# Performance work log

Hardware: AMD Instinct MI355X
Metric: run time of the kernel (lower is better)

## Reference

```python
import jax, jax.numpy as jnp
import numpy as np

VOCAB = 31      # 29 label chars + EOS('$') + PAD('%')
EMB = 512
KEY_DIM = 512
VAL_DIM = 512
HID = 512
T_ENC = 16384
MAX_LEN = 100
EOS_IDX = 29
PAD_IDX = 30


def setup_inputs() -> dict:
    key = jax.random.key(0)
    ks = jax.random.split(key, 9)
    inp = {
        "encoding": jax.random.normal(ks[0], (1, T_ENC, KEY_DIM + VAL_DIM), jnp.float32),
        "encoding_lens": jnp.array([T_ENC], dtype=jnp.int64),
        # learned parameters
        "embed": jax.random.normal(ks[1], (VOCAB, EMB), jnp.float32) * 0.02,
        "w_ih": jax.random.normal(ks[2], (3 * HID, EMB), jnp.float32) / np.sqrt(EMB),
        "w_hh": jax.random.normal(ks[3], (3 * HID, HID), jnp.float32) / np.sqrt(HID),
        "b_ih": jax.random.normal(ks[4], (3 * HID,), jnp.float32) * 0.01,
        "b_hh": jax.random.normal(ks[5], (3 * HID,), jnp.float32) * 0.01,
        "w_out": jax.random.normal(ks[6], (VOCAB, VAL_DIM + HID), jnp.float32) / np.sqrt(VAL_DIM + HID),
        "b_out": jax.random.normal(ks[7], (VOCAB,), jnp.float32) * 0.01,
    }
    return inp


def _gru_cell(x, h, w_ih, w_hh, b_ih, b_hh):
    # torch.nn.GRUCell math. x: [B,E], h: [B,H]
    gx = x @ w_ih.T + b_ih            # [B,3H]
    gh = h @ w_hh.T + b_hh            # [B,3H]
    r = jax.nn.sigmoid(gx[:, :HID] + gh[:, :HID])
    z = jax.nn.sigmoid(gx[:, HID:2 * HID] + gh[:, HID:2 * HID])
    n = jnp.tanh(gx[:, 2 * HID:] + r * gh[:, 2 * HID:])
    return (1.0 - z) * n + z * h


def reference(encoding, encoding_lens, embed, w_ih, w_hh, b_ih, b_hh, w_out, b_out):
    # batch_size == 1 inference path
    keys = encoding[0, :, :KEY_DIM]     # [T, K]
    values = encoding[0, :, KEY_DIM:]   # [T, V]
    # mask: positions whose key features are not all equal to the pad index
    mask = jnp.any(keys != jnp.float32(PAD_IDX), axis=-1)  # [T]
    scale = 1.0 / np.sqrt(KEY_DIM)

    y0 = embed[EOS_IDX][None, :]        # [1, E]
    h0 = jnp.zeros((1, HID), jnp.float32)

    def step(carry, _):
        y_prev, h = carry
        h_new = _gru_cell(y_prev, h, w_ih, w_hh, b_ih, b_hh)          # [1,H]
        scores = (h_new @ keys.T) * scale                              # [1,T]
        scores = jnp.where(mask[None, :], scores, jnp.float32(-1e9))
        attn = jax.nn.softmax(scores, axis=-1)                         # [1,T]
        summary = attn @ values                                        # [1,V]
        logits = jnp.concatenate([summary, h_new], axis=-1) @ w_out.T + b_out  # [1,VOCAB]
        best = jnp.argmax(logits, axis=-1)                             # [1] (softmax argmax == logits argmax)
        y_next = embed[best]                                           # [1,E]
        return (y_next, h_new), (logits[0], attn[0], best[0])

    _, (outputs, attentions, best_seq) = jax.lax.scan(step, (y0, h0), None, length=MAX_LEN)
    # emulate the early-exit: length = index of first EOS (outputs[:t] in torch), else MAX_LEN
    eos_hit = best_seq == EOS_IDX
    length = jnp.where(eos_hit.any(), jnp.argmax(eos_hit), MAX_LEN).astype(jnp.int32)
    return outputs[None, :, :], length[None], attentions[None, :, :]
```

## Files before the change

kernel.cpp:

```cpp
#include <hip/hip_runtime.h>
#include <math.h>

#define HID 512
#define TENC 16384
#define NBLK 256
#define TPB 512
#define KPB 64
#define NGRP 32
#define GRPSZ 8
#define VOCAB 31
#define EOSI 29
#define MAXLEN 100
#define SCALE 0.044194173824159216f

#define WS_GX    0
#define WS_GH    47616
#define WS_LT    50688
#define WS_BAR   51504

#define OUT_LEN_IDX 3100
#define OUT_ATT_BASE 3101

#define AL(p)    __hip_atomic_load((p), __ATOMIC_RELAXED, __HIP_MEMORY_SCOPE_AGENT)
#define AS(p, v) __hip_atomic_store((p), (v), __ATOMIC_RELAXED, __HIP_MEMORY_SCOPE_AGENT)

static __device__ __forceinline__ float wsum(float v) {
#pragma unroll
  for (int m = 32; m >= 1; m >>= 1) v += __shfl_xor(v, m, 64);
  return v;
}
static __device__ __forceinline__ float sigm(float x) { return 1.0f / (1.0f + expf(-x)); }

__global__ __launch_bounds__(1024) void k_init(const float* __restrict__ b_hh,
                                               float* __restrict__ ws) {
  int idx = blockIdx.x * 1024 + threadIdx.x;
  int* bars = (int*)ws + WS_BAR;
  if (idx < 12832) bars[idx] = 0;
  if (idx < 1536) ws[WS_GH + idx] = b_hh[idx];
  if (idx < 816) ws[WS_LT + idx] = 0.0f;
}

__global__ __launch_bounds__(256) void k_gx_all(const float* __restrict__ embed,
                                                const float* __restrict__ w_ih,
                                                const float* __restrict__ b_ih,
                                                float* __restrict__ ws) {
  int w = threadIdx.x >> 6, lane = threadIdx.x & 63;
  int r = blockIdx.x * 4 + w;
  float wr[8];
  const float* wp = w_ih + (size_t)r * HID + lane * 8;
#pragma unroll
  for (int j = 0; j < 8; ++j) wr[j] = wp[j];
  float b = b_ih[r];
  for (int v = 0; v < VOCAB; ++v) {
    const float* e = embed + (size_t)v * HID + lane * 8;
    float d = 0.f;
#pragma unroll
    for (int j = 0; j < 8; ++j) d += wr[j] * e[j];
    d = wsum(d);
    if (lane == 0) ws[WS_GX + v * 1536 + r] = d + b;
  }
}

static __device__ __forceinline__ void gridbar(int* bars, int t) {
  __syncthreads();
  int* cbase = bars + t * 128;
  int* epoch = bars + MAXLEN * 128;
  if (threadIdx.x == 0)
    __hip_atomic_fetch_add(cbase + (blockIdx.x & (NGRP - 1)) * 4, 1,
                           __ATOMIC_RELEASE, __HIP_MEMORY_SCOPE_AGENT);
  if (blockIdx.x == 0) {
    if (threadIdx.x < 64) {
      for (;;) {
        int c = AL(cbase + (threadIdx.x & 31) * 4);
        if (__all(c >= GRPSZ)) break;
        __builtin_amdgcn_s_sleep(1);
      }
      if (threadIdx.x < 8)
        __hip_atomic_store(epoch + threadIdx.x * 4, t + 1,
                           __ATOMIC_RELEASE, __HIP_MEMORY_SCOPE_AGENT);
    }
  } else {
    if (threadIdx.x == 0) {
      while (AL(epoch + (blockIdx.x & 7) * 4) < t + 1)
        __builtin_amdgcn_s_sleep(4);
    }
  }
  __syncthreads();
}

__global__ __launch_bounds__(TPB, 1) void k_persist(const float* __restrict__ enc,
                                                    const float* __restrict__ w_hh,
                                                    const float* __restrict__ b_hh,
                                                    const float* __restrict__ w_out,
                                                    const float* __restrict__ b_out,
                                                    float* __restrict__ ws,
                                                    float* __restrict__ dout) {
  const int tid = threadIdx.x, blk = blockIdx.x;
  const int w = tid >> 6, lane = tid & 63;
  __shared__ __align__(16) float k_lds[KPB][HID];
  __shared__ __align__(16) float h2[2][HID];
  __shared__ __align__(16) float uld[HID];
  __shared__ float sblk[KPB];
  __shared__ float okf[KPB];
  __shared__ float pb_lds[32];
  __shared__ float lgs[34];
  __shared__ float ered[8];
  int best = EOSI, len = MAXLEN;
  int* bars = (int*)ws + WS_BAR;

#pragma unroll
  for (int rr = 0; rr < 8; ++rr) {
    int r = w * 8 + rr;
    const float* rp = enc + (size_t)(blk * KPB + r) * 1024 + lane * 8;
    float4 k0 = *(const float4*)(rp);
    float4 k1 = *(const float4*)(rp + 4);
    *(float4*)&k_lds[r][lane * 8] = k0;
    *(float4*)&k_lds[r][lane * 8 + 4] = k1;
    bool okl = (k0.x != 30.f) || (k0.y != 30.f) || (k0.z != 30.f) || (k0.w != 30.f)
             || (k1.x != 30.f) || (k1.y != 30.f) || (k1.z != 30.f) || (k1.w != 30.f);
    bool ok = (__ballot(okl) != 0ull);
    if (lane == 0) okf[r] = ok ? 1.0f : 0.0f;
  }
  if (tid < HID) h2[0][tid] = 0.f;
  __syncthreads();

#pragma unroll 1
  for (int t = 0;; ++t) {
    float* h = h2[t & 1];
    float* hn = h2[(t + 1) & 1];

    if (t > 0) {
      const float* LT = ws + WS_LT + ((t - 1) % 3) * 272;
      if (tid < 64) {
        float val = 0.f;
        if (lane < VOCAB) {
#pragma unroll
          for (int s = 0; s < 8; ++s) val += AL(LT + s * 32 + lane);
        } else if (lane == 32) {
#pragma unroll
          for (int s = 0; s < 8; ++s) val += AL(LT + 256 + s);
        }
        float t1 = __shfl(val, 32, 64);
        if (lane < VOCAB) lgs[lane] = val / t1 + pb_lds[lane];
        if (lane == 32) lgs[32] = t1;
      }
      __syncthreads();
      float bv = lgs[0];
      int bb = 0;
#pragma unroll
      for (int v = 1; v < VOCAB; ++v) {
        float x = lgs[v];
        if (x > bv) { bv = x; bb = v; }
      }
      best = bb;
      if (bb == EOSI && len == MAXLEN) len = t - 1;
      float invT1 = 1.0f / lgs[32];
      if (tid < KPB)
        dout[OUT_ATT_BASE + (size_t)(t - 1) * TENC + blk * KPB + tid] = sblk[tid] * invT1;
      if (blk == 0) {
        if (tid < VOCAB) dout[(size_t)(t - 1) * VOCAB + tid] = lgs[tid];
        if (t == MAXLEN && tid == 0) dout[OUT_LEN_IDX] = (float)len;
        float* LTn = ws + WS_LT + ((t + 1) % 3) * 272;
        if (tid < 264) AS(LTn + tid, 0.0f);
      }
    }
    if (t == MAXLEN) break;

    {
      const float* gx = ws + WS_GX + best * 1536;
      const float* ghb = ws + WS_GH + (t & 1) * 1536;
      float gxr = gx[tid], gxz = gx[HID + tid], gxn = gx[2 * HID + tid];
      float ghr = AL(ghb + tid), ghz = AL(ghb + HID + tid), ghn = AL(ghb + 2 * HID + tid);
      float rg = sigm(gxr + ghr);
      float zg = sigm(gxz + ghz);
      float ng = tanhf(gxn + rg * ghn);
      hn[tid] = (1.f - zg) * ng + zg * h[tid];
      uld[tid] = 0.f;
    }
    __syncthreads();

    if (w < 6) {
      int r = blk * 6 + w;
      const float* wp = w_hh + (size_t)r * HID + lane * 8;
      float4 w0 = *(const float4*)(wp);
      float4 w1 = *(const float4*)(wp + 4);
      float4 hv0 = *(const float4*)(&hn[lane * 8]);
      float4 hv1 = *(const float4*)(&hn[lane * 8 + 4]);
      float acc = w0.x*hv0.x + w0.y*hv0.y + w0.z*hv0.z + w0.w*hv0.w
                + w1.x*hv1.x + w1.y*hv1.y + w1.z*hv1.z + w1.w*hv1.w;
      acc = wsum(acc);
      if (lane == 0) AS(ws + WS_GH + ((t + 1) & 1) * 1536 + r, acc + b_hh[r]);
    }

    float hr[8];
#pragma unroll
    for (int j = 0; j < 8; ++j) hr[j] = hn[lane * 8 + j];
    float4 v0[8], v1[8];
#pragma unroll
    for (int rr = 0; rr < 8; ++rr) {
      int row = blk * KPB + w * 8 + rr;
      const float* rp = enc + (size_t)row * 1024 + 512 + lane * 8;
      v0[rr] = *(const float4*)(rp);
      v1[rr] = *(const float4*)(rp + 4);
    }
    float ee[8];
    float esum = 0.f;
#pragma unroll
    for (int rr = 0; rr < 8; ++rr) {
      int r = w * 8 + rr;
      float4 k0 = *(const float4*)(&k_lds[r][lane * 8]);
      float4 k1 = *(const float4*)(&k_lds[r][lane * 8 + 4]);
      float d = hr[0]*k0.x + hr[1]*k0.y + hr[2]*k0.z + hr[3]*k0.w
              + hr[4]*k1.x + hr[5]*k1.y + hr[6]*k1.z + hr[7]*k1.w;
      float s = wsum(d);
      float e = okf[r] * __expf(s * SCALE);
      ee[rr] = e;
      if (lane == 0) sblk[r] = e;
      esum += e;
    }
    if (lane == 0) ered[w] = esum;
    {
      float ps[8] = {0, 0, 0, 0, 0, 0, 0, 0};
#pragma unroll
      for (int rr = 0; rr < 8; ++rr) {
        float e = ee[rr];
        ps[0] += e * v0[rr].x; ps[1] += e * v0[rr].y; ps[2] += e * v0[rr].z; ps[3] += e * v0[rr].w;
        ps[4] += e * v1[rr].x; ps[5] += e * v1[rr].y; ps[6] += e * v1[rr].z; ps[7] += e * v1[rr].w;
      }
#pragma unroll
      for (int j = 0; j < 8; ++j) atomicAdd(&uld[lane * 8 + j], ps[j]);
    }
    __syncthreads();
    if (tid == 0) {
      float T1p = ered[0] + ered[1] + ered[2] + ered[3]
                + ered[4] + ered[5] + ered[6] + ered[7];
      atomicAdd(ws + WS_LT + (t % 3) * 272 + 256 + (blk & 7), T1p);
    }

    for (int r = w; r < VOCAB; r += 8) {
      const float* wo = w_out + (size_t)r * 1024 + lane * 8;
      float4 a0 = *(const float4*)(wo);
      float4 a1 = *(const float4*)(wo + 4);
      float4 b0 = *(const float4*)(wo + 512);
      float4 b1 = *(const float4*)(wo + 516);
      float4 u0 = *(const float4*)(&uld[lane * 8]);
      float4 u1 = *(const float4*)(&uld[lane * 8 + 4]);
      float4 q0 = *(const float4*)(&hn[lane * 8]);
      float4 q1 = *(const float4*)(&hn[lane * 8 + 4]);
      float accs = a0.x*u0.x + a0.y*u0.y + a0.z*u0.z + a0.w*u0.w
                 + a1.x*u1.x + a1.y*u1.y + a1.z*u1.z + a1.w*u1.w;
      float acch = b0.x*q0.x + b0.y*q0.y + b0.z*q0.z + b0.w*q0.w
                 + b1.x*q1.x + b1.y*q1.y + b1.z*q1.z + b1.w*q1.w;
      accs = wsum(accs);
      acch = wsum(acch);
      if (lane == 0) {
        atomicAdd(ws + WS_LT + (t % 3) * 272 + (blk & 7) * 32 + r, accs);
        pb_lds[r] = acch + b_out[r];
      }
    }

    gridbar(bars, t);
  }
}

extern "C" void kernel_launch(void* const* d_in, const int* in_sizes, int n_in,
                              void* d_out, int out_size, void* d_ws, size_t ws_size,
                              hipStream_t stream) {
  const float* enc   = (const float*)d_in[0];
  const float* embed = (const float*)d_in[2];
  const float* w_ih  = (const float*)d_in[3];
  const float* w_hh  = (const float*)d_in[4];
  const float* b_ih  = (const float*)d_in[5];
  const float* b_hh  = (const float*)d_in[6];
  const float* w_out = (const float*)d_in[7];
  const float* b_out = (const float*)d_in[8];
  float* dout = (float*)d_out;
  float* ws = (float*)d_ws;

  hipLaunchKernelGGL(k_init, dim3(13), dim3(1024), 0, stream, b_hh, ws);
  hipLaunchKernelGGL(k_gx_all, dim3(384), dim3(256), 0, stream, embed, w_ih, b_ih, ws);
  hipLaunchKernelGGL(k_persist, dim3(NBLK), dim3(TPB), 0, stream,
                     enc, w_hh, b_hh, w_out, b_out, ws, dout);
}
```

Before: 2.764 ms.

## Keep values in registers, replace LDS atomics with per-wave reduction, widen barrier

Value rows are now loaded once into registers before the time loop instead of being re-read from global memory every step. The LDS atomicAdd accumulation of the attention summary is replaced by per-wave buffers summed by a plain reduction. Loads are reorganised into contiguous float4 lanes to avoid LDS bank conflicts. The grid barrier now publishes the epoch to 32 slots with a shorter sleep, and sigmoid/tanh use fast exp intrinsics. Holding 64 float4 of values in registers raises register pressure, and the extra syncthreads adds a small per-step cost.

```diff
diff --git a/kernel.cpp b/kernel.cpp
--- a/kernel.cpp
+++ b/kernel.cpp
@@ -29,13 +29,16 @@
   for (int m = 32; m >= 1; m >>= 1) v += __shfl_xor(v, m, 64);
   return v;
 }
-static __device__ __forceinline__ float sigm(float x) { return 1.0f / (1.0f + expf(-x)); }
+static __device__ __forceinline__ float sigm(float x) { return 1.0f / (1.0f + __expf(-x)); }
+static __device__ __forceinline__ float ftanh(float x) {
+  return 1.0f - 2.0f / (__expf(2.0f * x) + 1.0f);
+}
 
 __global__ __launch_bounds__(1024) void k_init(const float* __restrict__ b_hh,
                                                float* __restrict__ ws) {
   int idx = blockIdx.x * 1024 + threadIdx.x;
   int* bars = (int*)ws + WS_BAR;
-  if (idx < 12832) bars[idx] = 0;
+  if (idx < 12928) bars[idx] = 0;
   if (idx < 1536) ws[WS_GH + idx] = b_hh[idx];
   if (idx < 816) ws[WS_LT + idx] = 0.0f;
 }
@@ -66,23 +69,22 @@
   int* cbase = bars + t * 128;
   int* epoch = bars + MAXLEN * 128;
   if (threadIdx.x == 0)
-    __hip_atomic_fetch_add(cbase + (blockIdx.x & (NGRP - 1)) * 4, 1,
+    __hip_atomic_fetch_add(cbase + (blockIdx.x & 31) * 4, 1,
                            __ATOMIC_RELEASE, __HIP_MEMORY_SCOPE_AGENT);
   if (blockIdx.x == 0) {
-    if (threadIdx.x < 64) {
+    if (threadIdx.x < 32) {
       for (;;) {
-        int c = AL(cbase + (threadIdx.x & 31) * 4);
+        int c = AL(cbase + threadIdx.x * 4);
         if (__all(c >= GRPSZ)) break;
         __builtin_amdgcn_s_sleep(1);
       }
-      if (threadIdx.x < 8)
-        __hip_atomic_store(epoch + threadIdx.x * 4, t + 1,
-                           __ATOMIC_RELEASE, __HIP_MEMORY_SCOPE_AGENT);
+      __hip_atomic_store(epoch + threadIdx.x * 4, t + 1,
+                         __ATOMIC_RELEASE, __HIP_MEMORY_SCOPE_AGENT);
     }
   } else {
     if (threadIdx.x == 0) {
-      while (AL(epoch + (blockIdx.x & 7) * 4) < t + 1)
-        __builtin_amdgcn_s_sleep(4);
+      while (AL(epoch + (blockIdx.x & 31) * 4) < t + 1)
+        __builtin_amdgcn_s_sleep(2);
     }
   }
   __syncthreads();
@@ -98,6 +100,7 @@
   const int tid = threadIdx.x, blk = blockIdx.x;
   const int w = tid >> 6, lane = tid & 63;
   __shared__ __align__(16) float k_lds[KPB][HID];
+  __shared__ __align__(16) float uwave[8][HID];
   __shared__ __align__(16) float h2[2][HID];
   __shared__ __align__(16) float uld[HID];
   __shared__ float sblk[KPB];
@@ -108,14 +111,17 @@
   int best = EOSI, len = MAXLEN;
   int* bars = (int*)ws + WS_BAR;
 
+  float4 v0[8], v1[8];
 #pragma unroll
   for (int rr = 0; rr < 8; ++rr) {
     int r = w * 8 + rr;
-    const float* rp = enc + (size_t)(blk * KPB + r) * 1024 + lane * 8;
-    float4 k0 = *(const float4*)(rp);
-    float4 k1 = *(const float4*)(rp + 4);
-    *(float4*)&k_lds[r][lane * 8] = k0;
-    *(float4*)&k_lds[r][lane * 8 + 4] = k1;
+    const float* rp = enc + (size_t)(blk * KPB + r) * 1024;
+    float4 k0 = *(const float4*)(rp + lane * 4);
+    float4 k1 = *(const float4*)(rp + 256 + lane * 4);
+    v0[rr] = *(const float4*)(rp + 512 + lane * 4);
+    v1[rr] = *(const float4*)(rp + 768 + lane * 4);
+    *(float4*)&k_lds[r][lane * 4] = k0;
+    *(float4*)&k_lds[r][256 + lane * 4] = k1;
     bool okl = (k0.x != 30.f) || (k0.y != 30.f) || (k0.z != 30.f) || (k0.w != 30.f)
              || (k1.x != 30.f) || (k1.y != 30.f) || (k1.z != 30.f) || (k1.w != 30.f);
     bool ok = (__ballot(okl) != 0ull);
@@ -157,9 +163,11 @@
       float invT1 = 1.0f / lgs[32];
       if (tid < KPB)
         dout[OUT_ATT_BASE + (size_t)(t - 1) * TENC + blk * KPB + tid] = sblk[tid] * invT1;
-      if (blk == 0) {
+      if (blk == 17) {
         if (tid < VOCAB) dout[(size_t)(t - 1) * VOCAB + tid] = lgs[tid];
         if (t == MAXLEN && tid == 0) dout[OUT_LEN_IDX] = (float)len;
+      }
+      if (blk == 9) {
         float* LTn = ws + WS_LT + ((t + 1) % 3) * 272;
         if (tid < 264) AS(LTn + tid, 0.0f);
       }
@@ -173,45 +181,35 @@
       float ghr = AL(ghb + tid), ghz = AL(ghb + HID + tid), ghn = AL(ghb + 2 * HID + tid);
       float rg = sigm(gxr + ghr);
       float zg = sigm(gxz + ghz);
-      float ng = tanhf(gxn + rg * ghn);
+      float ng = ftanh(gxn + rg * ghn);
       hn[tid] = (1.f - zg) * ng + zg * h[tid];
-      uld[tid] = 0.f;
     }
     __syncthreads();
 
     if (w < 6) {
       int r = blk * 6 + w;
-      const float* wp = w_hh + (size_t)r * HID + lane * 8;
-      float4 w0 = *(const float4*)(wp);
-      float4 w1 = *(const float4*)(wp + 4);
-      float4 hv0 = *(const float4*)(&hn[lane * 8]);
-      float4 hv1 = *(const float4*)(&hn[lane * 8 + 4]);
+      const float* wp = w_hh + (size_t)r * HID;
+      float4 w0 = *(const float4*)(wp + lane * 4);
+      float4 w1 = *(const float4*)(wp + 256 + lane * 4);
+      float4 hv0 = *(const float4*)(&hn[lane * 4]);
+      float4 hv1 = *(const float4*)(&hn[256 + lane * 4]);
       float acc = w0.x*hv0.x + w0.y*hv0.y + w0.z*hv0.z + w0.w*hv0.w
                 + w1.x*hv1.x + w1.y*hv1.y + w1.z*hv1.z + w1.w*hv1.w;
       acc = wsum(acc);
       if (lane == 0) AS(ws + WS_GH + ((t + 1) & 1) * 1536 + r, acc + b_hh[r]);
     }
 
-    float hr[8];
-#pragma unroll
-    for (int j = 0; j < 8; ++j) hr[j] = hn[lane * 8 + j];
-    float4 v0[8], v1[8];
-#pragma unroll
-    for (int rr = 0; rr < 8; ++rr) {
-      int row = blk * KPB + w * 8 + rr;
-      const float* rp = enc + (size_t)row * 1024 + 512 + lane * 8;
-      v0[rr] = *(const float4*)(rp);
-      v1[rr] = *(const float4*)(rp + 4);
-    }
+    float4 hv0 = *(const float4*)(&hn[lane * 4]);
+    float4 hv1 = *(const float4*)(&hn[256 + lane * 4]);
     float ee[8];
     float esum = 0.f;
 #pragma unroll
     for (int rr = 0; rr < 8; ++rr) {
       int r = w * 8 + rr;
-      float4 k0 = *(const float4*)(&k_lds[r][lane * 8]);
-      float4 k1 = *(const float4*)(&k_lds[r][lane * 8 + 4]);
-      float d = hr[0]*k0.x + hr[1]*k0.y + hr[2]*k0.z + hr[3]*k0.w
-              + hr[4]*k1.x + hr[5]*k1.y + hr[6]*k1.z + hr[7]*k1.w;
+      float4 k0 = *(const float4*)(&k_lds[r][lane * 4]);
+      float4 k1 = *(const float4*)(&k_lds[r][256 + lane * 4]);
+      float d = hv0.x*k0.x + hv0.y*k0.y + hv0.z*k0.z + hv0.w*k0.w
+              + hv1.x*k1.x + hv1.y*k1.y + hv1.z*k1.z + hv1.w*k1.w;
       float s = wsum(d);
       float e = okf[r] * __expf(s * SCALE);
       ee[rr] = e;
@@ -220,33 +218,40 @@
     }
     if (lane == 0) ered[w] = esum;
     {
-      float ps[8] = {0, 0, 0, 0, 0, 0, 0, 0};
+      float p0 = 0.f, p1 = 0.f, p2 = 0.f, p3 = 0.f;
+      float p4 = 0.f, p5 = 0.f, p6 = 0.f, p7 = 0.f;
 #pragma unroll
       for (int rr = 0; rr < 8; ++rr) {
         float e = ee[rr];
-        ps[0] += e * v0[rr].x; ps[1] += e * v0[rr].y; ps[2] += e * v0[rr].z; ps[3] += e * v0[rr].w;
-        ps[4] += e * v1[rr].x; ps[5] += e * v1[rr].y; ps[6] += e * v1[rr].z; ps[7] += e * v1[rr].w;
-      }
-#pragma unroll
-      for (int j = 0; j < 8; ++j) atomicAdd(&uld[lane * 8 + j], ps[j]);
+        p0 += e * v0[rr].x; p1 += e * v0[rr].y; p2 += e * v0[rr].z; p3 += e * v0[rr].w;
+        p4 += e * v1[rr].x; p5 += e * v1[rr].y; p6 += e * v1[rr].z; p7 += e * v1[rr].w;
+      }
+      *(float4*)&uwave[w][lane * 4] = make_float4(p0, p1, p2, p3);
+      *(float4*)&uwave[w][256 + lane * 4] = make_float4(p4, p5, p6, p7);
     }
     __syncthreads();
+    {
+      float a = uwave[0][tid] + uwave[1][tid] + uwave[2][tid] + uwave[3][tid]
+              + uwave[4][tid] + uwave[5][tid] + uwave[6][tid] + uwave[7][tid];
+      uld[tid] = a;
+    }
     if (tid == 0) {
       float T1p = ered[0] + ered[1] + ered[2] + ered[3]
                 + ered[4] + ered[5] + ered[6] + ered[7];
       atomicAdd(ws + WS_LT + (t % 3) * 272 + 256 + (blk & 7), T1p);
     }
+    __syncthreads();
 
     for (int r = w; r < VOCAB; r += 8) {
-      const float* wo = w_out + (size_t)r * 1024 + lane * 8;
-      float4 a0 = *(const float4*)(wo);
-      float4 a1 = *(const float4*)(wo + 4);
-      float4 b0 = *(const float4*)(wo + 512);
-      float4 b1 = *(const float4*)(wo + 516);
-      float4 u0 = *(const float4*)(&uld[lane * 8]);
-      float4 u1 = *(const float4*)(&uld[lane * 8 + 4]);
-      float4 q0 = *(const float4*)(&hn[lane * 8]);
-      float4 q1 = *(const float4*)(&hn[lane * 8 + 4]);
+      const float* wo = w_out + (size_t)r * 1024;
+      float4 a0 = *(const float4*)(wo + lane * 4);
+      float4 a1 = *(const float4*)(wo + 256 + lane * 4);
+      float4 b0 = *(const float4*)(wo + 512 + lane * 4);
+      float4 b1 = *(const float4*)(wo + 768 + lane * 4);
+      float4 u0 = *(const float4*)(&uld[lane * 4]);
+      float4 u1 = *(const float4*)(&uld[256 + lane * 4]);
+      float4 q0 = *(const float4*)(&hn[lane * 4]);
+      float4 q1 = *(const float4*)(&hn[256 + lane * 4]);
       float accs = a0.x*u0.x + a0.y*u0.y + a0.z*u0.z + a0.w*u0.w
                  + a1.x*u1.x + a1.y*u1.y + a1.z*u1.z + a1.w*u1.w;
       float acch = b0.x*q0.x + b0.y*q0.y + b0.z*q0.z + b0.w*q0.w
```

New measurement: 2.280 ms. 1.21x faster.
